# Performance work log

Hardware: AMD Instinct MI355X
Metric: run time of the kernel (lower is better)

The kernel has to match this reference:

```python
import math
import jax, jax.numpy as jnp
import numpy as np

S = 32.0
M1 = 1.0
M2 = 0.5
M3 = 0.0
MM = M2 * math.sin(math.pi - M2)
NUM_CLASSES = 100000
FEATURES = 512
BATCH = 512


def setup_inputs() -> dict:
    key = jax.random.key(0)
    k1, k2, k3 = jax.random.split(key, 3)
    inputs = jax.random.normal(k1, (BATCH, FEATURES), dtype=jnp.float32)
    labels = jax.random.randint(k2, (BATCH,), 0, NUM_CLASSES, dtype=jnp.int64)
    # xavier_uniform on [num_classes, features]
    limit = math.sqrt(6.0 / (NUM_CLASSES + FEATURES))
    weight = jax.random.uniform(k3, (NUM_CLASSES, FEATURES), minval=-limit, maxval=limit, dtype=jnp.float32)
    return {"inputs": inputs, "labels": labels, "weight": weight}


def reference(inputs, labels, weight):
    # L2 normalize (torch F.normalize uses eps=1e-12 clamp on norm)
    inp_n = inputs / jnp.maximum(jnp.linalg.norm(inputs, axis=1, keepdims=True), 1e-12)
    w_n = weight / jnp.maximum(jnp.linalg.norm(weight, axis=1, keepdims=True), 1e-12)
    cos_in = jnp.clip(inp_n @ w_n.T, -1.0 + 1e-6, 1.0 - 1e-6)  # [N, C]
    theta_in = jnp.arccos(cos_in)
    one_hot = jax.nn.one_hot(labels, NUM_CLASSES, dtype=cos_in.dtype)
    theta_out = theta_in + (theta_in * (M1 - 1.0) + M2) * one_hot
    cos_out = jnp.where(
        theta_out < math.pi,
        jnp.cos(theta_out) - M3 * one_hot,
        cos_in - MM * one_hot - M3 * one_hot,
    )
    outs = S * cos_out  # [N, C]
    # mean cross-entropy
    logp = jax.nn.log_softmax(outs, axis=1)
    n = jnp.arange(BATCH)
    loss = -jnp.mean(logp[n, labels])
    target_cos_in = cos_in[n, labels][:, None]
    target_theta_in = theta_in[n, labels][:, None]
    target_cos_out = cos_out[n, labels][:, None]
    return loss, outs, target_cos_in, target_theta_in, target_cos_out
```

## Files before the change

kernel.cpp:

```cpp
#include <hip/hip_runtime.h>
#include <stdint.h>

#define BATCH 512
#define FEAT 512
#define NCLS 100000
#define BM 128
#define BN 128
#define BK 64
#define NBLK_N 782
#define NCHUNK (NBLK_N * 2)
#define SCALE_S 32.0f
#define MARGIN 0.5f
#define MM_CONST 0.23971276930210156f
#define PI_F 3.14159265358979f

typedef unsigned int u32;
typedef unsigned short u16;
typedef __bf16 bf16x8 __attribute__((ext_vector_type(8)));
typedef float f32x4 __attribute__((ext_vector_type(4)));

__device__ __forceinline__ u16 f2bf(float f) {
  u32 u = __float_as_uint(f);
  u += 0x7fffu + ((u >> 16) & 1u);
  return (u16)(u >> 16);
}

__device__ __forceinline__ void async_copy16(const void* g, void* l) {
  __builtin_amdgcn_global_load_lds((const __attribute__((address_space(1))) u32*)g,
                                   (__attribute__((address_space(3))) u32*)l,
                                   16, 0, 0);
}

__device__ __forceinline__ float block_reduce_sum(float v, float* sbuf) {
  for (int off = 1; off < 64; off <<= 1) v += __shfl_xor(v, off, 64);
  int wid = threadIdx.x >> 6, lane = threadIdx.x & 63;
  __syncthreads();
  if (lane == 0) sbuf[wid] = v;
  __syncthreads();
  return sbuf[0] + sbuf[1] + sbuf[2] + sbuf[3];
}

__global__ __launch_bounds__(256) void norm_rows_kernel(const float* __restrict__ src,
                                                        u16* __restrict__ dst) {
  __shared__ float sbuf[4];
  int row = blockIdx.x;
  const float2* p = (const float2*)(src + (size_t)row * FEAT);
  float2 v = p[threadIdx.x];
  float ss = block_reduce_sum(v.x * v.x + v.y * v.y, sbuf);
  float inv = 1.0f / fmaxf(sqrtf(ss), 1e-12f);
  u16 a = f2bf(v.x * inv), b = f2bf(v.y * inv);
  ((u32*)(dst + (size_t)row * FEAT))[threadIdx.x] = (u32)a | ((u32)b << 16);
}

__global__ __launch_bounds__(256) void gemm_kernel(const u16* __restrict__ A,
                                                   const u16* __restrict__ B,
                                                   const int* __restrict__ labels,
                                                   float* __restrict__ outs,
                                                   float* __restrict__ partials) {
  __shared__ __align__(16) u16 sA[BM * BK];
  __shared__ __align__(16) u16 sB[BN * BK];
  __shared__ int sLab[BM];

  const int tid = threadIdx.x;
  const int lane = tid & 63;
  const int wid = tid >> 6;
  const int waveM = wid >> 1, waveN = wid & 1;
  const int bn = blockIdx.x, bm = blockIdx.y;
  const int quad = lane >> 4, l15 = lane & 15;

  if (tid < BM) sLab[tid] = labels[bm * BM + tid];

  int srow[4], scb[4];
#pragma unroll
  for (int rd = 0; rd < 4; ++rd) {
    int idx = rd * 256 + tid;
    int r = idx >> 3;
    srow[rd] = r;
    scb[rd] = (idx & 7) ^ (r & 7);
  }

  f32x4 acc[4][4] = {};

  for (int kt = 0; kt < FEAT / BK; ++kt) {
#pragma unroll
    for (int rd = 0; rd < 4; ++rd) {
      int r = srow[rd], cb = scb[rd];
      const u16* ga = A + (size_t)(bm * BM + r) * FEAT + kt * BK + cb * 8;
      int brow = bn * BN + r;
      if (brow >= NCLS) brow = NCLS - 1;
      const u16* gb = B + (size_t)brow * FEAT + kt * BK + cb * 8;
      int li = (rd * 256 + tid) * 8;
      async_copy16(ga, &sA[li]);
      async_copy16(gb, &sB[li]);
    }
    __syncthreads();
#pragma unroll
    for (int ks = 0; ks < 2; ++ks) {
      int j0 = ks * 4 + quad;
      bf16x8 aF[4], bF[4];
#pragma unroll
      for (int mi = 0; mi < 4; ++mi) {
        int r = waveM * 64 + mi * 16 + l15;
        aF[mi] = *(const bf16x8*)&sA[(r * 8 + (j0 ^ (r & 7))) * 8];
      }
#pragma unroll
      for (int ni = 0; ni < 4; ++ni) {
        int r = waveN * 64 + ni * 16 + l15;
        bF[ni] = *(const bf16x8*)&sB[(r * 8 + (j0 ^ (r & 7))) * 8];
      }
#pragma unroll
      for (int mi = 0; mi < 4; ++mi)
#pragma unroll
        for (int ni = 0; ni < 4; ++ni)
          acc[mi][ni] = __builtin_amdgcn_mfma_f32_16x16x32_bf16(aF[mi], bF[ni],
                                                                acc[mi][ni], 0, 0, 0);
    }
    __syncthreads();
  }

#pragma unroll
  for (int mi = 0; mi < 4; ++mi) {
#pragma unroll
    for (int reg = 0; reg < 4; ++reg) {
      int rloc = waveM * 64 + mi * 16 + quad * 4 + reg;
      int rg = bm * BM + rloc;
      int lab = sLab[rloc];
      float vals[4];
      float rmax = -1e30f;
#pragma unroll
      for (int ni = 0; ni < 4; ++ni) {
        int cg = bn * BN + waveN * 64 + ni * 16 + l15;
        float v = acc[mi][ni][reg];
        v = fminf(fmaxf(v, -1.0f + 1e-6f), 1.0f - 1e-6f);
        if (cg == lab) {
          float th = acosf(v) + MARGIN;
          v = (th < PI_F) ? cosf(th) : (v - MM_CONST);
        }
        v *= SCALE_S;
        if (cg < NCLS)
          outs[(size_t)rg * NCLS + cg] = v;
        else
          v = -1e30f;
        vals[ni] = v;
        rmax = fmaxf(rmax, v);
      }
#pragma unroll
      for (int off = 1; off < 16; off <<= 1) rmax = fmaxf(rmax, __shfl_xor(rmax, off, 64));
      float rsum = 0.f;
#pragma unroll
      for (int ni = 0; ni < 4; ++ni) rsum += __expf(vals[ni] - rmax);
#pragma unroll
      for (int off = 1; off < 16; off <<= 1) rsum += __shfl_xor(rsum, off, 64);
      if (l15 == 0) {
        float* p = partials + ((size_t)rg * NCHUNK + (bn * 2 + waveN)) * 2;
        p[0] = rmax;
        p[1] = rsum;
      }
    }
  }
}

__global__ __launch_bounds__(256) void combine_kernel(const float* __restrict__ partials,
                                                      const float* __restrict__ outs,
                                                      const int* __restrict__ labels,
                                                      float* __restrict__ loss_r) {
  int r = blockIdx.x, tid = threadIdx.x;
  const float* p = partials + (size_t)r * NCHUNK * 2;
  float m = -1e30f, l = 0.f;
  for (int i = tid; i < NCHUNK; i += 256) {
    float mi = p[2 * i], li = p[2 * i + 1];
    if (mi > m) { l = l * __expf(m - mi) + li; m = mi; }
    else l += li * __expf(mi - m);
  }
  for (int off = 1; off < 64; off <<= 1) {
    float mo = __shfl_xor(m, off, 64);
    float lo = __shfl_xor(l, off, 64);
    if (mo > m) { l = l * __expf(m - mo) + lo; m = mo; }
    else l += lo * __expf(mo - m);
  }
  __shared__ float sm[4], sl[4];
  int wv = tid >> 6, lane = tid & 63;
  if (lane == 0) { sm[wv] = m; sl[wv] = l; }
  __syncthreads();
  if (tid == 0) {
    for (int w = 1; w < 4; ++w) {
      float mo = sm[w], lo = sl[w];
      if (mo > m) { l = l * __expf(m - mo) + lo; m = mo; }
      else l += lo * __expf(mo - m);
    }
    float lse = m + logf(l);
    loss_r[r] = lse - outs[(size_t)r * NCLS + labels[r]];
  }
}

__global__ __launch_bounds__(256) void loss_kernel(const float* __restrict__ loss_r,
                                                   float* __restrict__ out0) {
  __shared__ float sbuf[4];
  float v = loss_r[threadIdx.x] + loss_r[threadIdx.x + 256];
  float s = block_reduce_sum(v, sbuf);
  if (threadIdx.x == 0) out0[0] = s * (1.0f / BATCH);
}

__global__ __launch_bounds__(256) void targets_kernel(const float* __restrict__ inputs,
                                                      const int* __restrict__ labels,
                                                      const float* __restrict__ weight,
                                                      float* __restrict__ tdst) {
  __shared__ float sbuf[4];
  int r = blockIdx.x, t = threadIdx.x;
  int lab = labels[r];
  const float2* px = (const float2*)(inputs + (size_t)r * FEAT);
  const float2* pw = (const float2*)(weight + (size_t)lab * FEAT);
  float2 x = px[t], w = pw[t];
  float dot = block_reduce_sum(x.x * w.x + x.y * w.y, sbuf);
  float sx = block_reduce_sum(x.x * x.x + x.y * x.y, sbuf);
  float sw = block_reduce_sum(w.x * w.x + w.y * w.y, sbuf);
  if (t == 0) {
    float inv = 1.0f / (fmaxf(sqrtf(sx), 1e-12f) * fmaxf(sqrtf(sw), 1e-12f));
    float ci = fminf(fmaxf(dot * inv, -1.0f + 1e-6f), 1.0f - 1e-6f);
    float th = acosf(ci);
    float t2 = th + MARGIN;
    float co = (t2 < PI_F) ? cosf(t2) : (ci - MM_CONST);
    tdst[r] = ci;
    tdst[BATCH + r] = th;
    tdst[2 * BATCH + r] = co;
  }
}

extern "C" void kernel_launch(void* const* d_in, const int* in_sizes, int n_in,
                              void* d_out, int out_size, void* d_ws, size_t ws_size,
                              hipStream_t stream) {
  const float* inputs = (const float*)d_in[0];
  const int* labels = (const int*)d_in[1];
  const float* weight = (const float*)d_in[2];
  float* out = (float*)d_out;
  float* outs = out + 1;
  float* tdst = out + 1 + (size_t)BATCH * NCLS;

  char* ws = (char*)d_ws;
  u16* wsA = (u16*)ws;
  u16* wsB = (u16*)(ws + 524288);
  float* partials = (float*)(ws + 524288 + 102400000);
  float* loss_r = (float*)(ws + 524288 + 102400000 + (size_t)BATCH * NCHUNK * 2 * 4);

  norm_rows_kernel<<<BATCH, 256, 0, stream>>>(inputs, wsA);
  norm_rows_kernel<<<NCLS, 256, 0, stream>>>(weight, wsB);
  gemm_kernel<<<dim3(NBLK_N, BATCH / BM), 256, 0, stream>>>(wsA, wsB, labels, outs, partials);
  combine_kernel<<<BATCH, 256, 0, stream>>>(partials, outs, labels, loss_r);
  loss_kernel<<<1, 256, 0, stream>>>(loss_r, out);
  targets_kernel<<<BATCH, 256, 0, stream>>>(inputs, labels, weight, tdst);
}
```

Baseline: 571.2 us.

## Double-buffer GEMM LDS tiles, remap blocks for locality, merge norm kernels

The GEMM now double-buffers its A/B LDS tiles, issuing the async global-to-LDS loads for the next K tile before computing the current one. It waits on a vmcnt count instead of a full sync, so load latency overlaps with MFMA work. A 1D grid with an XCD-aware block remap places the four M-blocks that share a B tile close together, to improve L2 reuse of weight rows. The two row-normalisation launches become one grid-stride kernel that uses one wave per row with float4 loads, removing a launch and the LDS reduction, at the cost of twice the GEMM LDS footprint.

```diff
diff --git a/kernel.cpp b/kernel.cpp
--- a/kernel.cpp
+++ b/kernel.cpp
@@ -8,6 +8,7 @@
 #define BN 128
 #define BK 64
 #define NBLK_N 782
+#define NBLK (NBLK_N * 4)
 #define NCHUNK (NBLK_N * 2)
 #define SCALE_S 32.0f
 #define MARGIN 0.5f
@@ -40,16 +41,39 @@
   return sbuf[0] + sbuf[1] + sbuf[2] + sbuf[3];
 }
 
-__global__ __launch_bounds__(256) void norm_rows_kernel(const float* __restrict__ src,
-                                                        u16* __restrict__ dst) {
-  __shared__ float sbuf[4];
-  int row = blockIdx.x;
-  const float2* p = (const float2*)(src + (size_t)row * FEAT);
-  float2 v = p[threadIdx.x];
-  float ss = block_reduce_sum(v.x * v.x + v.y * v.y, sbuf);
-  float inv = 1.0f / fmaxf(sqrtf(ss), 1e-12f);
-  u16 a = f2bf(v.x * inv), b = f2bf(v.y * inv);
-  ((u32*)(dst + (size_t)row * FEAT))[threadIdx.x] = (u32)a | ((u32)b << 16);
+__global__ __launch_bounds__(256) void norm_all_kernel(const float* __restrict__ inputs,
+                                                       const float* __restrict__ weight,
+                                                       u16* __restrict__ dstA,
+                                                       u16* __restrict__ dstB) {
+  const int lane = threadIdx.x & 63;
+  const int gw = (blockIdx.x * 256 + threadIdx.x) >> 6;
+  const int nw = gridDim.x * 4;
+  for (int row = gw; row < BATCH + NCLS; row += nw) {
+    const float* src;
+    u16* dst;
+    if (row < BATCH) {
+      src = inputs + (size_t)row * FEAT;
+      dst = dstA + (size_t)row * FEAT;
+    } else {
+      src = weight + (size_t)(row - BATCH) * FEAT;
+      dst = dstB + (size_t)(row - BATCH) * FEAT;
+    }
+    const float4* p4 = (const float4*)src;
+    float4 a = p4[lane];
+    float4 b = p4[lane + 64];
+    float ss = a.x * a.x + a.y * a.y + a.z * a.z + a.w * a.w +
+               b.x * b.x + b.y * b.y + b.z * b.z + b.w * b.w;
+#pragma unroll
+    for (int off = 1; off < 64; off <<= 1) ss += __shfl_xor(ss, off, 64);
+    float inv = 1.0f / fmaxf(sqrtf(ss), 1e-12f);
+    ushort4 oa, ob;
+    oa.x = f2bf(a.x * inv); oa.y = f2bf(a.y * inv);
+    oa.z = f2bf(a.z * inv); oa.w = f2bf(a.w * inv);
+    ob.x = f2bf(b.x * inv); ob.y = f2bf(b.y * inv);
+    ob.z = f2bf(b.z * inv); ob.w = f2bf(b.w * inv);
+    ((ushort4*)dst)[lane] = oa;
+    ((ushort4*)dst)[lane + 64] = ob;
+  }
 }
 
 __global__ __launch_bounds__(256) void gemm_kernel(const u16* __restrict__ A,
@@ -57,43 +81,58 @@
                                                    const int* __restrict__ labels,
                                                    float* __restrict__ outs,
                                                    float* __restrict__ partials) {
-  __shared__ __align__(16) u16 sA[BM * BK];
-  __shared__ __align__(16) u16 sB[BN * BK];
+  __shared__ __align__(16) u16 sA[2][BM * BK];
+  __shared__ __align__(16) u16 sB[2][BN * BK];
   __shared__ int sLab[BM];
 
   const int tid = threadIdx.x;
   const int lane = tid & 63;
   const int wid = tid >> 6;
   const int waveM = wid >> 1, waveN = wid & 1;
-  const int bn = blockIdx.x, bm = blockIdx.y;
+  const int orig = blockIdx.x;
+  const int L = (orig & 7) * (NBLK / 8) + (orig >> 3);
+  const int bm = L & 3, bn = L >> 2;
   const int quad = lane >> 4, l15 = lane & 15;
 
   if (tid < BM) sLab[tid] = labels[bm * BM + tid];
 
-  int srow[4], scb[4];
+  const u16* gA[4];
+  const u16* gB[4];
 #pragma unroll
   for (int rd = 0; rd < 4; ++rd) {
     int idx = rd * 256 + tid;
     int r = idx >> 3;
-    srow[rd] = r;
-    scb[rd] = (idx & 7) ^ (r & 7);
-  }
+    int cb = (idx & 7) ^ (r & 7);
+    gA[rd] = A + (size_t)(bm * BM + r) * FEAT + cb * 8;
+    int brow = bn * BN + r;
+    if (brow >= NCLS) brow = NCLS - 1;
+    gB[rd] = B + (size_t)brow * FEAT + cb * 8;
+  }
+
+#define STAGE(buf, kt)                                      \
+  do {                                                      \
+    _Pragma("unroll") for (int rd = 0; rd < 4; ++rd) {      \
+      int li = (rd * 256 + tid) * 8;                        \
+      async_copy16(gA[rd] + (kt)*BK, &sA[buf][li]);         \
+      async_copy16(gB[rd] + (kt)*BK, &sB[buf][li]);         \
+    }                                                       \
+  } while (0)
 
   f32x4 acc[4][4] = {};
 
+  STAGE(0, 0);
+  __syncthreads();
+
+  int cur = 0;
+#pragma unroll
   for (int kt = 0; kt < FEAT / BK; ++kt) {
-#pragma unroll
-    for (int rd = 0; rd < 4; ++rd) {
-      int r = srow[rd], cb = scb[rd];
-      const u16* ga = A + (size_t)(bm * BM + r) * FEAT + kt * BK + cb * 8;
-      int brow = bn * BN + r;
-      if (brow >= NCLS) brow = NCLS - 1;
-      const u16* gb = B + (size_t)brow * FEAT + kt * BK + cb * 8;
-      int li = (rd * 256 + tid) * 8;
-      async_copy16(ga, &sA[li]);
-      async_copy16(gb, &sB[li]);
-    }
-    __syncthreads();
+    if (kt < FEAT / BK - 1) {
+      STAGE(cur ^ 1, kt + 1);
+      asm volatile("s_waitcnt vmcnt(8)" ::: "memory");
+    } else {
+      asm volatile("s_waitcnt vmcnt(0)" ::: "memory");
+    }
+    asm volatile("s_barrier" ::: "memory");
 #pragma unroll
     for (int ks = 0; ks < 2; ++ks) {
       int j0 = ks * 4 + quad;
@@ -101,12 +140,12 @@
 #pragma unroll
       for (int mi = 0; mi < 4; ++mi) {
         int r = waveM * 64 + mi * 16 + l15;
-        aF[mi] = *(const bf16x8*)&sA[(r * 8 + (j0 ^ (r & 7))) * 8];
+        aF[mi] = *(const bf16x8*)&sA[cur][(r * 8 + (j0 ^ (r & 7))) * 8];
       }
 #pragma unroll
       for (int ni = 0; ni < 4; ++ni) {
         int r = waveN * 64 + ni * 16 + l15;
-        bF[ni] = *(const bf16x8*)&sB[(r * 8 + (j0 ^ (r & 7))) * 8];
+        bF[ni] = *(const bf16x8*)&sB[cur][(r * 8 + (j0 ^ (r & 7))) * 8];
       }
 #pragma unroll
       for (int mi = 0; mi < 4; ++mi)
@@ -115,8 +154,10 @@
           acc[mi][ni] = __builtin_amdgcn_mfma_f32_16x16x32_bf16(aF[mi], bF[ni],
                                                                 acc[mi][ni], 0, 0, 0);
     }
-    __syncthreads();
-  }
+    asm volatile("s_barrier" ::: "memory");
+    cur ^= 1;
+  }
+#undef STAGE
 
 #pragma unroll
   for (int mi = 0; mi < 4; ++mi) {
@@ -242,9 +283,8 @@
   float* partials = (float*)(ws + 524288 + 102400000);
   float* loss_r = (float*)(ws + 524288 + 102400000 + (size_t)BATCH * NCHUNK * 2 * 4);
 
-  norm_rows_kernel<<<BATCH, 256, 0, stream>>>(inputs, wsA);
-  norm_rows_kernel<<<NCLS, 256, 0, stream>>>(weight, wsB);
-  gemm_kernel<<<dim3(NBLK_N, BATCH / BM), 256, 0, stream>>>(wsA, wsB, labels, outs, partials);
+  norm_all_kernel<<<2048, 256, 0, stream>>>(inputs, weight, wsA, wsB);
+  gemm_kernel<<<NBLK, 256, 0, stream>>>(wsA, wsB, labels, outs, partials);
   combine_kernel<<<BATCH, 256, 0, stream>>>(partials, outs, labels, loss_r);
   loss_kernel<<<1, 256, 0, stream>>>(loss_r, out);
   targets_kernel<<<BATCH, 256, 0, stream>>>(inputs, labels, weight, tdst);
```

Measured after the change: 561.0 us. Within noise of the previous version (-1.8%).
